# Performance work log

Measured on AMD Instinct MI355X. Metric: run time of the kernel, lower is better.

The kernel has to match this reference:

```python
import itertools
import jax, jax.numpy as jnp
import numpy as np

# ---- static config (mirrors args) ----
BS = 4; NUM_SEM = 24; C = 4 + NUM_SEM
H_SCREEN = 240; W_SCREEN = 320
FOV = 60.0
RES = 5; Z_RES = 5
MAP_SIZE_CM = 4800 // 2            # global_downscaling = 2
MAP_CELLS = MAP_SIZE_CM // RES     # 480
VR = 100                           # vision_range
AGENT_HEIGHT = 1.55 * 100.0        # cm
MAX_H = int(360 / Z_RES)           # 72
MIN_H = int(-40 / Z_RES)           # -8
MAP_PRED_THR = 1.0; EXP_PRED_THR = 1.0; CAT_PRED_THR = 5.0
SHIFT_X = VR * RES // 2            # 250 cm (shift_loc)
XC = (W_SCREEN - 1.0) / 2.0
ZC = (H_SCREEN - 1.0) / 2.0
FOCAL = (W_SCREEN / 2.0) / float(np.tan(np.deg2rad(FOV / 2.0)))
DEG2RAD = float(np.pi / 180.0)
R2D = 57.29577951308232


def splat_feat_nd(init_grid, feat, coords):
    # init_grid [B,F,D0,D1,D2], feat [B,F,N], coords [B,3,N] in [-1,1]
    B, Fc = init_grid.shape[0], init_grid.shape[1]
    dims = init_grid.shape[2:]
    grid_flat = init_grid.reshape(B, Fc, -1)
    pos_all, wts_all = [], []
    for d in range(len(dims)):
        Dd = dims[d]
        pos = coords[:, d, :] * (Dd / 2.0) + Dd / 2.0   # [B,N]
        fl = jnp.floor(pos)
        pd, wd = [], []
        for off in (0.0, 1.0):
            p = fl + off
            safe = ((p > 0) & (p < Dd)).astype(pos.dtype)
            wd.append((1.0 - jnp.abs(pos - p)) * safe)
            pd.append(p * safe)
        pos_all.append(pd); wts_all.append(wd)
    bidx = jnp.arange(B)[:, None, None]
    fidx = jnp.arange(Fc)[None, :, None]
    for corner in itertools.product((0, 1), repeat=len(dims)):
        index = jnp.zeros_like(pos_all[0][0])
        wts = jnp.ones_like(pos_all[0][0])
        for d in range(len(dims)):
            index = index * dims[d] + pos_all[d][corner[d]]
            wts = wts * wts_all[d][corner[d]]
        idx = index.astype(jnp.int32)[:, None, :]        # [B,1,N]
        grid_flat = grid_flat.at[bidx, fidx, idx].add(feat * wts[:, None, :])
    return jnp.round(grid_flat).reshape(init_grid.shape)


def affine_grid(theta, H, W):
    # align_corners=True base grid; theta [B,2,3] -> grid [B,H,W,2]
    xs = jnp.linspace(-1.0, 1.0, W)
    ys = jnp.linspace(-1.0, 1.0, H)
    gx, gy = jnp.meshgrid(xs, ys)                        # [H,W]
    base = jnp.stack([gx, gy, jnp.ones_like(gx)], axis=-1)
    return jnp.einsum('hwk,bjk->bhwj', base, theta)


def grid_sample(img, grid):
    # bilinear, zero padding, align_corners=True. img [B,C,H,W], grid [B,Ho,Wo,2]
    B, Cc, H, W = img.shape
    ix = (grid[..., 0] + 1.0) * 0.5 * (W - 1)
    iy = (grid[..., 1] + 1.0) * 0.5 * (H - 1)
    x0 = jnp.floor(ix); y0 = jnp.floor(iy)
    x1 = x0 + 1.0; y1 = y0 + 1.0
    wx1 = ix - x0; wx0 = 1.0 - wx1
    wy1 = iy - y0; wy0 = 1.0 - wy1
    bidx = jnp.arange(B)[:, None, None]
    def gather(xi, yi):
        valid = ((xi >= 0) & (xi <= W - 1) & (yi >= 0) & (yi <= H - 1)).astype(img.dtype)
        xc = jnp.clip(xi, 0, W - 1).astype(jnp.int32)
        yc = jnp.clip(yi, 0, H - 1).astype(jnp.int32)
        v = img[bidx, :, yc, xc]                          # [B,Ho,Wo,C]
        return v * valid[..., None]
    out = (gather(x0, y0) * (wx0 * wy0)[..., None]
           + gather(x1, y0) * (wx1 * wy0)[..., None]
           + gather(x0, y1) * (wx0 * wy1)[..., None]
           + gather(x1, y1) * (wx1 * wy1)[..., None])
    return jnp.transpose(out, (0, 3, 1, 2))


def setup_inputs():
    key = jax.random.key(0)
    k1, k2, k3, k4, k5, k6, k7 = jax.random.split(key, 7)
    rgb = jax.random.uniform(k1, (BS, 3, H_SCREEN, W_SCREEN), jnp.float32)
    depth = jax.random.uniform(k2, (BS, 1, H_SCREEN, W_SCREEN), jnp.float32, 50.0, 500.0)  # cm
    seg = jax.random.uniform(k3, (BS, NUM_SEM, H_SCREEN, W_SCREEN), jnp.float32)
    obs = jnp.concatenate([rgb, depth, seg], axis=1)
    pose_obs = jax.random.uniform(k4, (BS, 3), jnp.float32, -0.1, 0.1)
    maps_last = jax.random.uniform(k5, (BS, C, MAP_CELLS, MAP_CELLS), jnp.float32)
    xy = jax.random.uniform(k6, (BS, 2), jnp.float32, 8.0, 16.0)   # meters, inside map
    th = jax.random.uniform(k7, (BS, 1), jnp.float32, -180.0, 180.0)
    poses_last = jnp.concatenate([xy, th], axis=1)
    view_angles = jnp.zeros((BS,), jnp.float32)
    return {"obs": obs, "pose_obs": pose_obs, "maps_last": maps_last,
            "poses_last": poses_last, "view_angles": view_angles, "holding_state": 0}


def _forward(obs, pose_obs, maps_last, poses_last, view_angles):
    bs, c, h, w = obs.shape
    # holding_state == 0 path: mask_err_below = depth < 0
    depth = jnp.where(obs[:, 3] < 0.0, 1e4, obs[:, 3])
    # point cloud from depth (du_scale == 1)
    x_idx = jnp.arange(w, dtype=depth.dtype)
    z_idx = jnp.arange(h - 1, -1, -1).astype(depth.dtype)
    X = (x_idx[None, None, :] - XC) * depth / FOCAL
    Z = (z_idx[None, :, None] - ZC) * depth / FOCAL
    XYZ = jnp.stack([X, depth, Z], axis=-1)              # [bs,h,w,3]
    # camera elevation rotation about x-axis, then add sensor height
    a = view_angles * DEG2RAD
    ca, sa = jnp.cos(a), jnp.sin(a)
    z0 = jnp.zeros_like(ca); o1 = jnp.ones_like(ca)
    Rx = jnp.stack([o1, z0, z0, z0, ca, -sa, z0, sa, ca], -1).reshape(bs, 3, 3)
    XYZ = jnp.einsum('bij,bhwj->bhwi', Rx, XYZ)
    XYZ = XYZ.at[..., 2].add(AGENT_HEIGHT)
    # transform_pose_t with shift_loc: z-rotation by pi/2-pi/2=0, +x shift
    XYZ = XYZ.at[..., 0].add(float(SHIFT_X))
    # normalize to [-1,1] voxel coords
    xy_n = (XYZ[..., :2] / RES - VR // 2.0) / VR * 2.0
    z_n = (XYZ[..., 2] / Z_RES - (MAX_H + MIN_H) // 2.0) / (MAX_H - MIN_H) * 2.0
    coords = jnp.concatenate([xy_n, z_n[..., None]], axis=-1)
    coords = coords.reshape(bs, h * w, 3).transpose(0, 2, 1)            # [bs,3,N]
    feat = jnp.concatenate([jnp.ones((bs, 1, h * w), obs.dtype),
                            obs[:, 4:].reshape(bs, c - 4, h * w)], axis=1)
    init_grid = jnp.zeros((bs, 1 + NUM_SEM, VR, VR, MAX_H - MIN_H), obs.dtype)
    voxels = splat_feat_nd(init_grid, feat, coords).transpose(0, 1, 3, 2, 4)
    min_z = int(15 / Z_RES - MIN_H)
    max_z = int((AGENT_HEIGHT + 1 + 50) / Z_RES - MIN_H)
    agent_height_proj = voxels[..., min_z:max_z].sum(-1)
    all_height_proj = voxels.sum(-1)
    fp_map_pred = jnp.clip(agent_height_proj[:, 0:1] / MAP_PRED_THR, 0.0, 1.0)
    fp_exp_pred = jnp.clip(all_height_proj[:, 0:1] / EXP_PRED_THR, 0.0, 1.0)
    x1 = MAP_CELLS // 2 - VR // 2; x2 = x1 + VR
    y1 = MAP_CELLS // 2; look = VR - 4; y2 = y1 + look
    agent_view = jnp.zeros((bs, c, MAP_CELLS, MAP_CELLS), obs.dtype)
    agent_view = agent_view.at[:, 0:1, y1:y2, x1:x2].set(fp_map_pred[:, :, :look, :])
    agent_view = agent_view.at[:, 1:2, y1:y2, x1:x2].set(fp_exp_pred[:, :, :look, :])
    agent_view = agent_view.at[:, 4:, y1:y2, x1:x2].set(
        jnp.clip(agent_height_proj[:, 1:] / CAT_PRED_THR, 0.0, 1.0)[:, :, :look, :])
    # pose composition (get_new_pose_batch)
    th0 = poses_last[:, 2] / R2D
    ny = poses_last[:, 1] + pose_obs[:, 0] * jnp.sin(th0) + pose_obs[:, 1] * jnp.cos(th0)
    nx = poses_last[:, 0] + pose_obs[:, 0] * jnp.cos(th0) - pose_obs[:, 1] * jnp.sin(th0)
    no = poses_last[:, 2] + pose_obs[:, 2] * R2D
    no = jnp.fmod(no - 180.0, 360.0) + 180.0
    no = jnp.fmod(no + 180.0, 360.0) - 180.0
    current_poses = jnp.stack([nx, ny, no], axis=1)
    st = jax.lax.stop_gradient(current_poses)            # st_pose is .detach()ed
    half = MAP_CELLS // 2
    sx = -(st[:, 0] * 100.0 / RES - half) / half
    sy = -(st[:, 1] * 100.0 / RES - half) / half
    t = (90.0 - st[:, 2]) * DEG2RAD
    ct, s_t = jnp.cos(t), jnp.sin(t)
    zz = jnp.zeros_like(ct); oo = jnp.ones_like(ct)
    theta_rot = jnp.stack([ct, -s_t, zz, s_t, ct, zz], -1).reshape(bs, 2, 3)
    theta_tr = jnp.stack([oo, zz, sx, zz, oo, sy], -1).reshape(bs, 2, 3)
    rot_grid = affine_grid(theta_rot, MAP_CELLS, MAP_CELLS)
    trans_grid = affine_grid(theta_tr, MAP_CELLS, MAP_CELLS)
    rotated = grid_sample(agent_view, rot_grid)
    translated = grid_sample(rotated, trans_grid)
    map_pred = jnp.maximum(maps_last, translated)        # torch.max over stacked pair
    return fp_map_pred, map_pred, current_poses, current_poses


def reference(obs, pose_obs, maps_last, poses_last, view_angles, holding_state):
    # holding_state == 0 path (no object held); branches for 1/2 are host-side numpy.
    return _forward(obs, pose_obs, maps_last, poses_last, view_angles)
```

## Files before the change

### kernel.cpp

```cpp
#include <hip/hip_runtime.h>
#include <math.h>

#define BS 4
#define CC 28
#define NF 25
#define HS 240
#define WSC 320
#define NPIX (HS*WSC)
#define VR 100
#define ZD 80
#define MC 480
#define NCELL (VR*VR)
#define NREC_MAX ((size_t)BS*NPIX*4)
#define NSTRIP 8192
#define ROWS 28
#define FSTR 32
#define SBMAX 159

__device__ __forceinline__ float clip01(float v){ return fminf(fmaxf(v, 0.f), 1.f); }

struct Geo {
    float wx[2], wy[2], wz[2];
    int   xi[2], yi[2], zi[2];
    bool  sx[2], sy[2];
};

__device__ __forceinline__ Geo compute_geo(const float* __restrict__ obs,
                                           const float* __restrict__ view_angles,
                                           int b, int pix){
    int j = pix % WSC;
    int i = pix / WSC;
    float depth = obs[((size_t)(b*CC + 3))*NPIX + pix];
    if (depth < 0.f) depth = 10000.f;
    const float FOCAL = 277.12812921102035f;
    float X = ((float)j - 159.5f) * depth / FOCAL;
    float Z = ((float)(HS-1-i) - 119.5f) * depth / FOCAL;
    float a = view_angles[b] * 0.017453292519943295f;
    float ca = cosf(a), sa = sinf(a);
    float Y2 = ca*depth - sa*Z;
    float Z2 = sa*depth + ca*Z + 155.f;
    float X2 = X + 250.f;

    float px = ((X2/5.f - 50.f)/100.f*2.f)*50.f + 50.f;
    float py = ((Y2/5.f - 50.f)/100.f*2.f)*50.f + 50.f;
    float pz = ((Z2/5.f - 32.f)/80.f*2.f)*40.f + 40.f;

    Geo g;
    float fx = floorf(px), fy = floorf(py), fz = floorf(pz);
    {
        float p0 = fx, p1 = fx + 1.f;
        g.sx[0] = (p0 > 0.f) && (p0 < 100.f);
        g.sx[1] = (p1 > 0.f) && (p1 < 100.f);
        g.wx[0] = g.sx[0] ? (1.f - fabsf(px - p0)) : 0.f;
        g.wx[1] = g.sx[1] ? (1.f - fabsf(px - p1)) : 0.f;
        g.xi[0] = g.sx[0] ? (int)p0 : 0;
        g.xi[1] = g.sx[1] ? (int)p1 : 0;
    }
    {
        float p0 = fy, p1 = fy + 1.f;
        g.sy[0] = (p0 > 0.f) && (p0 < 100.f);
        g.sy[1] = (p1 > 0.f) && (p1 < 100.f);
        g.wy[0] = g.sy[0] ? (1.f - fabsf(py - p0)) : 0.f;
        g.wy[1] = g.sy[1] ? (1.f - fabsf(py - p1)) : 0.f;
        g.yi[0] = g.sy[0] ? (int)p0 : 0;
        g.yi[1] = g.sy[1] ? (int)p1 : 0;
    }
    {
        float p0 = fz, p1 = fz + 1.f;
        bool s0 = (p0 > 0.f) && (p0 < 80.f);
        bool s1 = (p1 > 0.f) && (p1 < 80.f);
        g.wz[0] = s0 ? (1.f - fabsf(pz - p0)) : 0.f;
        g.wz[1] = s1 ? (1.f - fabsf(pz - p1)) : 0.f;
        g.zi[0] = s0 ? (int)p0 : 0;
        g.zi[1] = s1 ? (int)p1 : 0;
    }
    return g;
}

__global__ void pose_kernel(const float* __restrict__ pose_obs,
                            const float* __restrict__ poses_last,
                            float* __restrict__ out_p1,
                            float* __restrict__ out_p2,
                            float* __restrict__ params){
    int b = threadIdx.x;
    if (b >= BS) return;
    const float R2D = 57.29577951308232f;
    float th0 = poses_last[b*3+2] / R2D;
    float s0 = sinf(th0), c0 = cosf(th0);
    float ny = poses_last[b*3+1] + pose_obs[b*3+0]*s0 + pose_obs[b*3+1]*c0;
    float nx = poses_last[b*3+0] + pose_obs[b*3+0]*c0 - pose_obs[b*3+1]*s0;
    float no = poses_last[b*3+2] + pose_obs[b*3+2]*R2D;
    no = fmodf(no - 180.f, 360.f) + 180.f;
    no = fmodf(no + 180.f, 360.f) - 180.f;
    out_p1[b*3+0] = nx; out_p1[b*3+1] = ny; out_p1[b*3+2] = no;
    out_p2[b*3+0] = nx; out_p2[b*3+1] = ny; out_p2[b*3+2] = no;
    const float half = 240.f;
    float sx = -(nx*100.f/5.f - half)/half;
    float sy = -(ny*100.f/5.f - half)/half;
    float t = (90.f - no) * 0.017453292519943295f;
    params[b*4+0] = cosf(t);
    params[b*4+1] = sinf(t);
    params[b*4+2] = sx;
    params[b*4+3] = sy;
}

__global__ __launch_bounds__(256)
void prep_kernel(const float* __restrict__ obs,
                 const float* __restrict__ view_angles,
                 int* __restrict__ counts,
                 float* __restrict__ feat){
    __shared__ float sf[6400];
    int t   = threadIdx.x;
    int tid = blockIdx.x * 256 + t;
    int b   = tid / NPIX;
    int pix = tid % NPIX;

    Geo g = compute_geo(obs, view_angles, b, pix);
    #pragma unroll
    for (int cy = 0; cy < 2; ++cy)
    #pragma unroll
    for (int cx = 0; cx < 2; ++cx){
        if (g.sx[cx] && g.sy[cy] && (g.wx[cx]*g.wy[cy] != 0.f))
            atomicAdd(&counts[b*NCELL + g.yi[cy]*VR + g.xi[cx]], 1);
    }

    #pragma unroll 6
    for (int f = 0; f < 24; ++f)
        sf[t*25 + f] = obs[((size_t)(b*CC + 4 + f))*NPIX + pix];
    __syncthreads();
    size_t base = ((size_t)b*NPIX + (size_t)(pix - t)) * FSTR;
    for (int q = t; q < 256*FSTR; q += 256){
        int pl = q >> 5, ff = q & 31;
        feat[base + q] = (ff < 24) ? sf[pl*25 + ff] : 0.f;
    }
}

__global__ void scan_kernel(const int* __restrict__ counts,
                            int* __restrict__ bases,
                            int* __restrict__ cursor,
                            int* __restrict__ cell_start){
    __shared__ int partC[1024], partW[1024];
    int t = threadIdx.x;
    const int TOT = BS*NCELL;
    const int CH  = 40;
    int beg = t*CH;
    int sc = 0, sw = 0;
    for (int i = 0; i < CH; ++i){
        int idx = beg + i;
        if (idx < TOT){ int c = counts[idx]; sc += c; sw += c + (c ? 24 : 6); }
    }
    partC[t] = sc; partW[t] = sw;
    __syncthreads();
    for (int off = 1; off < 1024; off <<= 1){
        int vc = (t >= off) ? partC[t-off] : 0;
        int vw = (t >= off) ? partW[t-off] : 0;
        __syncthreads();
        partC[t] += vc; partW[t] += vw;
        __syncthreads();
    }
    int totw  = partW[1023];
    int quota = (totw + NSTRIP - 1) / NSTRIP;
    if (quota < 1) quota = 1;
    int runC = (t == 0) ? 0 : partC[t-1];
    int runW = (t == 0) ? 0 : partW[t-1];
    if (t == 0) cell_start[0] = 0;
    for (int i = 0; i < CH; ++i){
        int idx = beg + i;
        if (idx >= TOT) break;
        int c = counts[idx];
        bases[idx]  = runC;
        cursor[idx] = runC;
        int w = c + (c ? 24 : 6);
        int sCur = runW / quota; if (sCur > NSTRIP-1) sCur = NSTRIP-1;
        runC += c; runW += w;
        int sNext = runW / quota; if (sNext > NSTRIP-1) sNext = NSTRIP-1;
        if (idx == TOT-1){
            bases[TOT] = runC;
            for (int gg = sCur+1; gg <= NSTRIP; ++gg) cell_start[gg] = TOT;
        } else {
            for (int gg = sCur+1; gg <= sNext; ++gg) cell_start[gg] = idx+1;
        }
    }
}

__global__ __launch_bounds__(256)
void scatter_kernel(const float* __restrict__ obs,
                    const float* __restrict__ view_angles,
                    int* __restrict__ cursor,
                    uint4* __restrict__ records){
    int tid = blockIdx.x * 256 + threadIdx.x;
    int b   = tid / NPIX;
    int pix = tid % NPIX;
    Geo g = compute_geo(obs, view_angles, b, pix);
    #pragma unroll
    for (int cy = 0; cy < 2; ++cy)
    #pragma unroll
    for (int cx = 0; cx < 2; ++cx){
        float wxy = g.wx[cx] * g.wy[cy];
        if (g.sx[cx] && g.sy[cy] && (wxy != 0.f)){
            int cid = b*NCELL + g.yi[cy]*VR + g.xi[cx];
            int pos = atomicAdd(&cursor[cid], 1);
            float w0 = wxy * g.wz[0];
            float w1 = wxy * g.wz[1];
            unsigned iw = (unsigned)pix | ((unsigned)g.zi[0] << 17)
                                        | ((unsigned)g.zi[1] << 24);
            records[pos] = make_uint4(__float_as_uint(w0), __float_as_uint(w1), iw, 0u);
        }
    }
}


#define GATHERV(V, SUB) \
  _Pragma("unroll") \
  for (int u = 0; u < 8; ++u){ \
    int idx = (SUB) + 2*u + rr; \
    V[u] = 1.f; \
    if (flane && idx < n && f != 0){ \
      int pixq = (int)(srec[idx].z & 0x1FFFFu); \
      V[u] = feat_b[(size_t)pixq*FSTR + (f-1)]; } }

#define FLUSHV(V, SUB) \
  _Pragma("unroll") \
  for (int u = 0; u < 8; ++u){ \
    int idx = (SUB) + 2*u + rr; \
    if (flane && idx < n){ \
      uint4 rv = srec[idx]; \
      float w0 = __uint_as_float(rv.x), w1 = __uint_as_float(rv.y); \
      int z0 = (int)((rv.z >> 17) & 0x7Fu); \
      int z1 = (int)((rv.z >> 24) & 0x7Fu); \
      if (w0 != 0.f) atomicAdd(&col[z0*NF + f], V[u]*w0); \
      if (w1 != 0.f) atomicAdd(&col[z1*NF + f], V[u]*w1); } }

__global__ __launch_bounds__(64)
void accum_kernel(const uint4* __restrict__ records,
                  const float* __restrict__ feat,
                  const int* __restrict__ bases,
                  const int* __restrict__ cell_start,
                  float* __restrict__ ahp,
                  float* __restrict__ out0){
    __shared__ float col[ZD*NF];
    __shared__ uint4 srec[64];
    __shared__ int   sb[SBMAX+1];

    int g0 = blockIdx.x;
    int g  = (g0 & 7)*(NSTRIP/8) + (g0 >> 3);
    int t  = threadIdx.x;
    int c0 = cell_start[g];
    int c1 = cell_start[g+1];
    int nc = c1 - c0;
    if (nc <= 0) return;
    if (nc > SBMAX) nc = SBMAX;
    int f  = t & 31;
    int rr = t >> 5;
    bool flane = (f < NF);

    for (int i = t; i <= nc; i += 64) sb[i] = bases[c0 + i];
    {   float4* c4 = (float4*)col;
        #pragma unroll
        for (int i = 0; i < 8; ++i){ int idx = t + i*64; if (idx < 500) c4[idx] = make_float4(0,0,0,0); } }

    const uint4 Zq = make_uint4(0u,0u,0u,0u);
    uint4 cur = Zq;
    bool pf = false;

    for (int ci = 0; ci < nc; ++ci){
        int start = sb[ci], end = sb[ci+1];
        int cid = c0 + ci;
        if (start >= end){
            float* row = ahp + (size_t)cid*ROWS;
            if (t < ROWS) row[t] = 0.f;
            if (t == 0)  out0[cid] = 0.f;
            continue;
        }
        int b = cid / NCELL;
        const float* feat_b = feat + (size_t)b*NPIX*FSTR;

        if (!pf){
            int n0 = end - start; if (n0 > 64) n0 = 64;
            cur = (t < n0) ? records[start + t] : Zq;
        }
        pf = false;

        for (int cb = start; cb < end; cb += 64){
            int n = end - cb; if (n > 64) n = 64;
            srec[t] = cur;
            if (cb + 64 < end){
                int n2 = end - cb - 64; if (n2 > 64) n2 = 64;
                cur = (t < n2) ? records[cb + 64 + t] : Zq;
            } else if (ci + 1 < nc){
                int s2 = sb[ci+1], e2 = sb[ci+2];
                if (s2 < e2){
                    int n2 = e2 - s2; if (n2 > 64) n2 = 64;
                    cur = (t < n2) ? records[s2 + t] : Zq;
                    pf = true;
                }
            }
            float vA[8], vB[8];
            GATHERV(vA, 0);
            for (int sub = 0; sub < n; ){
                int nx = sub + 16;
                if (nx < n) GATHERV(vB, nx);
                FLUSHV(vA, sub);
                sub = nx; if (sub >= n) break;
                nx = sub + 16;
                if (nx < n) GATHERV(vA, nx);
                FLUSHV(vB, sub);
                sub = nx;
            }
        }

        {
            int f2 = t % NF, q = t / NF;
            float sall = 0.f, sag = 0.f;
            if (t < 50){
                for (int z = q*40; z < q*40 + 40; ++z){
                    float rv = rintf(col[z*NF + f2]);
                    sall += rv;
                    if (z >= 11 && z < 49) sag += rv;
                }
            }
            float sall_o = __shfl(sall, (t + 25) & 63, 64);
            float sag_o  = __shfl(sag,  (t + 25) & 63, 64);
            float* row = ahp + (size_t)cid*ROWS;
            if (t < NF){
                float a = sag + sag_o;
                float s = sall + sall_o;
                row[t] = a;
                if (t == 0){
                    row[25] = s;
                    out0[cid] = clip01(a);
                }
            } else if (t == 26 || t == 27){
                row[t] = 0.f;
            }
        }
        {   float4* c4 = (float4*)col;
            #pragma unroll
            for (int i = 0; i < 8; ++i){ int idx = t + i*64; if (idx < 500) c4[idx] = make_float4(0,0,0,0); } }
    }
}

__global__ __launch_bounds__(256)
void final_kernel(const float* __restrict__ ahp,
                  const float* __restrict__ params,
                  const float* __restrict__ maps_last,
                  float* __restrict__ out1){
    int tid = blockIdx.x * blockDim.x + threadIdx.x;
    if (tid >= BS*MC*MC) return;
    int w = tid % MC;
    int h = (tid / MC) % MC;
    int b = tid / (MC*MC);

    float ct = params[b*4+0], st = params[b*4+1];
    float sx = params[b*4+2], sy = params[b*4+3];

    float gx = -1.f + 2.f*(float)w/479.f;
    float gy = -1.f + 2.f*(float)h/479.f;
    float ix = (gx + sx + 1.f)*0.5f*479.f;
    float iy = (gy + sy + 1.f)*0.5f*479.f;
    float x0 = floorf(ix), y0 = floorf(iy);
    float wx1 = ix - x0, wx0 = 1.f - wx1;
    float wy1 = iy - y0, wy0 = 1.f - wy1;

    int   offs[16];
    float wt16[16];
    int nz = 0;
    #pragma unroll
    for (int tc = 0; tc < 4; ++tc){
        float txf = (tc & 1) ? x0 + 1.f : x0;
        float tyf = (tc & 2) ? y0 + 1.f : y0;
        float wt  = ((tc & 1) ? wx1 : wx0) * ((tc & 2) ? wy1 : wy0);
        bool validT = (txf >= 0.f) && (txf <= 479.f) && (tyf >= 0.f) && (tyf <= 479.f);
        int txc = (int)fminf(fmaxf(txf, 0.f), 479.f);
        int tyc = (int)fminf(fmaxf(tyf, 0.f), 479.f);

        float gx2 = -1.f + 2.f*(float)txc/479.f;
        float gy2 = -1.f + 2.f*(float)tyc/479.f;
        float rgx = ct*gx2 - st*gy2;
        float rgy = st*gx2 + ct*gy2;
        float ixr = (rgx + 1.f)*0.5f*479.f;
        float iyr = (rgy + 1.f)*0.5f*479.f;
        float rx0 = floorf(ixr), ry0 = floorf(iyr);
        float rwx1 = ixr - rx0, rwx0 = 1.f - rwx1;
        float rwy1 = iyr - ry0, rwy0 = 1.f - rwy1;

        #pragma unroll
        for (int rc = 0; rc < 4; ++rc){
            int id = tc*4 + rc;
            float rxf = (rc & 1) ? rx0 + 1.f : rx0;
            float ryf = (rc & 2) ? ry0 + 1.f : ry0;
            float wr  = ((rc & 1) ? rwx1 : rwx0) * ((rc & 2) ? rwy1 : rwy0);
            bool validR = (rxf >= 0.f) && (rxf <= 479.f) && (ryf >= 0.f) && (ryf <= 479.f);
            int rxc = (int)fminf(fmaxf(rxf, 0.f), 479.f);
            int ryc = (int)fminf(fmaxf(ryf, 0.f), 479.f);
            bool inwin = validT && validR &&
                         (rxc >= 190) && (rxc < 290) && (ryc >= 240) && (ryc < 336);
            float wgt = wt * wr;
            if (inwin && wgt != 0.f){
                offs[id] = (ryc - 240)*VR + (rxc - 190);
                wt16[id] = wgt;
                nz++;
            } else {
                offs[id] = -1;
                wt16[id] = 0.f;
            }
        }
    }

    size_t outBase = (size_t)b*CC*MC*MC + (size_t)h*MC + w;
    if (nz == 0){
        #pragma unroll
        for (int ch = 0; ch < CC; ++ch){
            size_t o = outBase + (size_t)ch*MC*MC;
            out1[o] = fmaxf(maps_last[o], 0.f);
        }
        return;
    }

    const float* ahp_b = ahp + (size_t)b*NCELL*ROWS;
    float acc[26];
    #pragma unroll
    for (int k = 0; k < 26; ++k) acc[k] = 0.f;

    #pragma unroll
    for (int id = 0; id < 16; ++id){
        if (offs[id] < 0) continue;
        float v[28];
        {
            const float4* rp = (const float4*)(ahp_b + (size_t)offs[id]*ROWS);
            #pragma unroll
            for (int k = 0; k < 7; ++k){
                float4 r = rp[k];
                v[4*k]   = r.x; v[4*k+1] = r.y;
                v[4*k+2] = r.z; v[4*k+3] = r.w;
            }
        }
        float wgt = wt16[id];
        acc[0] += wgt * clip01(v[0]);
        acc[1] += wgt * clip01(v[25]);
        #pragma unroll
        for (int ff = 1; ff < 25; ++ff)
            acc[1+ff] += wgt * clip01(v[ff] / 5.f);
    }

    #pragma unroll
    for (int ch = 0; ch < CC; ++ch){
        float a;
        if (ch == 0)      a = acc[0];
        else if (ch == 1) a = acc[1];
        else if (ch < 4)  a = 0.f;
        else              a = acc[ch-2];
        size_t o = outBase + (size_t)ch*MC*MC;
        out1[o] = fmaxf(maps_last[o], a);
    }
}

extern "C" void kernel_launch(void* const* d_in, const int* in_sizes, int n_in,
                              void* d_out, int out_size, void* d_ws, size_t ws_size,
                              hipStream_t stream){
    const float* obs         = (const float*)d_in[0];
    const float* pose_obs    = (const float*)d_in[1];
    const float* maps_last   = (const float*)d_in[2];
    const float* poses_last  = (const float*)d_in[3];
    const float* view_angles = (const float*)d_in[4];
    float* out = (float*)d_out;

    const size_t OUT0 = (size_t)BS*VR*VR;
    const size_t OUT1 = (size_t)BS*CC*MC*MC;
    float* out0 = out;
    float* out1 = out + OUT0;
    float* out2 = out + OUT0 + OUT1;
    float* out3 = out2 + BS*3;

    const size_t AHP_FLOATS  = (size_t)BS*NCELL*ROWS;
    const size_t NCID        = (size_t)BS*NCELL;
    const size_t FEAT_FLOATS = (size_t)BS*NPIX*FSTR;
    const size_t CS_INTS     = NSTRIP + 1;

    float* ahp    = (float*)d_ws;
    float* params = ahp + AHP_FLOATS;
    char*  ws_tail = (char*)(params + 16);
    size_t ws_used_small = (size_t)(ws_tail - (char*)d_ws);

    const size_t BIG_BYTES = (NCID*3 + 1 + CS_INTS)*4 + 64 + NREC_MAX*16 + FEAT_FLOATS*4;
    char* big;
    if (ws_size >= ws_used_small + BIG_BYTES){
        big = ws_tail;
    } else {
        big = (char*)(out1 + OUT1) - BIG_BYTES;
        big = (char*)((uintptr_t)big & ~(uintptr_t)15);
    }
    int* counts     = (int*)big;
    int* bases      = counts + NCID;
    int* cursor     = bases + NCID + 1;
    int* cell_start = cursor + NCID;
    uint4* records = (uint4*)(((uintptr_t)(cell_start + CS_INTS) + 15) & ~(uintptr_t)15);
    float* feat    = (float*)(records + NREC_MAX);

    hipMemsetAsync(counts, 0, NCID*4, stream);
    pose_kernel<<<1, 64, 0, stream>>>(pose_obs, poses_last, out2, out3, params);

    int nblk = (BS*NPIX)/256;
    prep_kernel<<<nblk, 256, 0, stream>>>(obs, view_angles, counts, feat);
    scan_kernel<<<1, 1024, 0, stream>>>(counts, bases, cursor, cell_start);
    scatter_kernel<<<nblk, 256, 0, stream>>>(obs, view_angles, cursor, records);
    accum_kernel<<<NSTRIP, 64, 0, stream>>>(records, feat, bases, cell_start,
                                            ahp, out0);
    final_kernel<<<(BS*MC*MC + 255)/256, 256, 0, stream>>>(ahp, params,
                                                           maps_last, out1);
}
```

Baseline: 866.1 us.

## Broadcast splat records via readlane instead of LDS staging in accum kernel

The accumulation kernel no longer stages each 64-record batch in shared memory. Lanes now pull record fields straight from registers with readlane, four records per iteration, two per half-wave. The cross-cell prefetch and the 8-deep gather/flush software pipeline are replaced by a simpler per-cell next-batch prefetch. This removes LDS writes and reads for records, but fewer feature gathers are in flight at once, which can expose global-memory latency.

```diff
diff --git a/kernel.cpp b/kernel.cpp
--- a/kernel.cpp
+++ b/kernel.cpp
@@ -18,6 +18,9 @@
 #define SBMAX 159
 
 __device__ __forceinline__ float clip01(float v){ return fminf(fmaxf(v, 0.f), 1.f); }
+__device__ __forceinline__ unsigned rl(unsigned v, int k){
+    return (unsigned)__builtin_amdgcn_readlane((int)v, k);
+}
 
 struct Geo {
     float wx[2], wy[2], wz[2];
@@ -209,28 +212,6 @@
     }
 }
 
-
-#define GATHERV(V, SUB) \
-  _Pragma("unroll") \
-  for (int u = 0; u < 8; ++u){ \
-    int idx = (SUB) + 2*u + rr; \
-    V[u] = 1.f; \
-    if (flane && idx < n && f != 0){ \
-      int pixq = (int)(srec[idx].z & 0x1FFFFu); \
-      V[u] = feat_b[(size_t)pixq*FSTR + (f-1)]; } }
-
-#define FLUSHV(V, SUB) \
-  _Pragma("unroll") \
-  for (int u = 0; u < 8; ++u){ \
-    int idx = (SUB) + 2*u + rr; \
-    if (flane && idx < n){ \
-      uint4 rv = srec[idx]; \
-      float w0 = __uint_as_float(rv.x), w1 = __uint_as_float(rv.y); \
-      int z0 = (int)((rv.z >> 17) & 0x7Fu); \
-      int z1 = (int)((rv.z >> 24) & 0x7Fu); \
-      if (w0 != 0.f) atomicAdd(&col[z0*NF + f], V[u]*w0); \
-      if (w1 != 0.f) atomicAdd(&col[z1*NF + f], V[u]*w1); } }
-
 __global__ __launch_bounds__(64)
 void accum_kernel(const uint4* __restrict__ records,
                   const float* __restrict__ feat,
@@ -239,7 +220,6 @@
                   float* __restrict__ ahp,
                   float* __restrict__ out0){
     __shared__ float col[ZD*NF];
-    __shared__ uint4 srec[64];
     __shared__ int   sb[SBMAX+1];
 
     int g0 = blockIdx.x;
@@ -260,8 +240,6 @@
         for (int i = 0; i < 8; ++i){ int idx = t + i*64; if (idx < 500) c4[idx] = make_float4(0,0,0,0); } }
 
     const uint4 Zq = make_uint4(0u,0u,0u,0u);
-    uint4 cur = Zq;
-    bool pf = false;
 
     for (int ci = 0; ci < nc; ++ci){
         int start = sb[ci], end = sb[ci+1];
@@ -275,38 +253,55 @@
         int b = cid / NCELL;
         const float* feat_b = feat + (size_t)b*NPIX*FSTR;
 
-        if (!pf){
-            int n0 = end - start; if (n0 > 64) n0 = 64;
-            cur = (t < n0) ? records[start + t] : Zq;
-        }
-        pf = false;
-
-        for (int cb = start; cb < end; cb += 64){
-            int n = end - cb; if (n > 64) n = 64;
-            srec[t] = cur;
-            if (cb + 64 < end){
-                int n2 = end - cb - 64; if (n2 > 64) n2 = 64;
-                cur = (t < n2) ? records[cb + 64 + t] : Zq;
-            } else if (ci + 1 < nc){
-                int s2 = sb[ci+1], e2 = sb[ci+2];
-                if (s2 < e2){
-                    int n2 = e2 - s2; if (n2 > 64) n2 = 64;
-                    cur = (t < n2) ? records[s2 + t] : Zq;
-                    pf = true;
+        int cb = start;
+        int n  = end - start; if (n > 64) n = 64;
+        uint4 cur = (t < n) ? records[start + t] : Zq;
+
+        while (cb < end){
+            int nb = cb + 64;
+            uint4 nxt = Zq; int n2 = 0;
+            if (nb < end){
+                n2 = end - nb; if (n2 > 64) n2 = 64;
+                nxt = (t < n2) ? records[nb + t] : Zq;
+            }
+
+            for (int k = 0; k < n; k += 4){
+                int p1 = (k+1 < n) ? k+1 : k;  bool pv1 = (k+1 < n);
+                int q0 = (k+2 < n) ? k+2 : k;  bool qv0 = (k+2 < n);
+                int q1 = (k+3 < n) ? k+3 : k;  bool qv1 = (k+3 < n);
+
+                unsigned pxa = rl(cur.x,k),  pya = rl(cur.y,k),  pza = rl(cur.z,k);
+                unsigned pxb = rl(cur.x,p1), pyb = rl(cur.y,p1), pzb = rl(cur.z,p1);
+                if (!pv1){ pxb = 0u; pyb = 0u; }
+                unsigned qxa = rl(cur.x,q0), qya = rl(cur.y,q0), qza = rl(cur.z,q0);
+                if (!qv0){ qxa = 0u; qya = 0u; }
+                unsigned qxb = rl(cur.x,q1), qyb = rl(cur.y,q1), qzb = rl(cur.z,q1);
+                if (!qv1){ qxb = 0u; qyb = 0u; }
+
+                float    pw0 = __uint_as_float(rr ? pxb : pxa);
+                float    pw1 = __uint_as_float(rr ? pyb : pya);
+                unsigned piw = rr ? pzb : pza;
+                float    qw0 = __uint_as_float(rr ? qxb : qxa);
+                float    qw1 = __uint_as_float(rr ? qyb : qya);
+                unsigned qiw = rr ? qzb : qza;
+
+                int ppix = (int)(piw & 0x1FFFFu);
+                int qpix = (int)(qiw & 0x1FFFFu);
+
+                float pval = 1.f, qval = 1.f;
+                if (flane && f != 0){
+                    pval = feat_b[(size_t)ppix*FSTR + (f-1)];
+                    qval = feat_b[(size_t)qpix*FSTR + (f-1)];
+                }
+                if (flane){
+                    int z;
+                    z = (int)((piw >> 17) & 0x7Fu); if (pw0 != 0.f) atomicAdd(&col[z*NF + f], pval*pw0);
+                    z = (int)((piw >> 24) & 0x7Fu); if (pw1 != 0.f) atomicAdd(&col[z*NF + f], pval*pw1);
+                    z = (int)((qiw >> 17) & 0x7Fu); if (qw0 != 0.f) atomicAdd(&col[z*NF + f], qval*qw0);
+                    z = (int)((qiw >> 24) & 0x7Fu); if (qw1 != 0.f) atomicAdd(&col[z*NF + f], qval*qw1);
                 }
             }
-            float vA[8], vB[8];
-            GATHERV(vA, 0);
-            for (int sub = 0; sub < n; ){
-                int nx = sub + 16;
-                if (nx < n) GATHERV(vB, nx);
-                FLUSHV(vA, sub);
-                sub = nx; if (sub >= n) break;
-                nx = sub + 16;
-                if (nx < n) GATHERV(vA, nx);
-                FLUSHV(vB, sub);
-                sub = nx;
-            }
+            cur = nxt; n = n2; cb = nb;
         }
 
         {
```

New measurement: 849.3 us. No clear change (-1.9%).
